# Performance work log

Measured on AMD Instinct MI355X. Metric: run time of the kernel, lower is better.

Reference implementation:

```python
import jax, jax.numpy as jnp
import numpy as np

VOCAB, EMB, HID = 32000, 256, 512
B, S = 16, 256


def setup_inputs() -> dict:
    key = jax.random.key(0)
    ks = jax.random.split(key, 7)
    x = jax.random.randint(ks[0], (B, S), 0, VOCAB, dtype=jnp.int32)
    E = jax.random.normal(ks[1], (VOCAB, EMB), dtype=jnp.float32) * 0.02
    # GRUCell kernels, gate order [z, r, h], reset_after=True (keras default)
    W = jax.random.normal(ks[2], (EMB, 3 * HID), dtype=jnp.float32) * 0.02
    U = jax.random.normal(ks[3], (HID, 3 * HID), dtype=jnp.float32) * 0.02
    b = jnp.zeros((2, 3 * HID), dtype=jnp.float32)  # [input_bias, recurrent_bias]
    Wd = jax.random.normal(ks[4], (HID, VOCAB), dtype=jnp.float32) * 0.02
    bd = jnp.zeros((VOCAB,), dtype=jnp.float32)
    return {"x": x, "E": E, "W": W, "U": U, "b": b, "Wd": Wd, "bd": bd}


def _gru_sequence(emb, W, U, b):
    # emb: [B, S, EMB]. Precompute all input-side gate projections at once.
    xw = jnp.einsum('bse,eh->bsh', emb, W) + b[0]          # [B, S, 3H]
    xw_t = jnp.transpose(xw, (1, 0, 2))                     # [S, B, 3H]
    b_rec = b[1]
    H = U.shape[0]

    def step(h, xt):
        rec = h @ U + b_rec                                 # [B, 3H]
        xz, xr, xh = xt[:, :H], xt[:, H:2 * H], xt[:, 2 * H:]
        rz, rr, rh = rec[:, :H], rec[:, H:2 * H], rec[:, 2 * H:]
        z = jax.nn.sigmoid(xz + rz)
        r = jax.nn.sigmoid(xr + rr)
        hh = jnp.tanh(xh + r * rh)                          # reset_after=True form
        h_new = z * h + (1.0 - z) * hh
        return h_new, h_new

    h0 = jnp.zeros((emb.shape[0], H), dtype=emb.dtype)
    _, hs = jax.lax.scan(step, h0, xw_t)                    # hs: [S, B, H]
    return jnp.transpose(hs, (1, 0, 2))                     # [B, S, H]


def reference(x, E, W, U, b, Wd, bd):
    emb = E[x]                                              # [B, S, EMB]
    h = _gru_sequence(emb, W, U, b)                         # [B, S, H]
    logits = jnp.einsum('bsh,hv->bsv', h, Wd) + bd          # [B, S, VOCAB]
    return logits
```

## Files before the change

kernel.cpp:

```cpp
#include <hip/hip_runtime.h>
#include <hip/hip_bf16.h>
#include <stdint.h>
#include <stddef.h>

#define NB 16
#define NS 256
#define NH 512
#define NE 256
#define NV 32000
#define NM (NB*NS)
#define N3H 1536

typedef __attribute__((ext_vector_type(8))) short short8v;
typedef __attribute__((ext_vector_type(4))) float float4v;
typedef __attribute__((address_space(1))) const unsigned int gas_u32;
typedef __attribute__((address_space(3))) unsigned int las_u32;

static __device__ __forceinline__ unsigned short f2bf(float f) {
  __hip_bfloat16 h = __float2bfloat16(f);
  return *reinterpret_cast<unsigned short*>(&h);
}
static __device__ __forceinline__ float bf2f(unsigned short u) {
  union { unsigned int u; float f; } c;
  c.u = ((unsigned int)u) << 16;
  return c.f;
}
static __device__ __forceinline__ float fast_tanh(float x) {
  float t = __expf(2.f * x);
  return (t - 1.f) / (t + 1.f);
}

__global__ void gather_emb(const int* __restrict__ x, const float* __restrict__ E,
                           unsigned short* __restrict__ A) {
  int m = blockIdx.x * 4 + (threadIdx.x >> 6);
  int lane = threadIdx.x & 63;
  int t = x[m];
  float4 v = reinterpret_cast<const float4*>(E + (size_t)t * NE)[lane];
  ushort4 o = make_ushort4(f2bf(v.x), f2bf(v.y), f2bf(v.z), f2bf(v.w));
  reinterpret_cast<ushort4*>(A + (size_t)m * NE)[lane] = o;
}

template<typename T>
__global__ void transpose_conv(const float* __restrict__ in, T* __restrict__ out,
                               int R, int C) {
  __shared__ float tile[32][33];
  int c0 = blockIdx.x * 32, r0 = blockIdx.y * 32;
  int tx = threadIdx.x, ty = threadIdx.y;
  #pragma unroll
  for (int i = 0; i < 32; i += 8)
    tile[ty + i][tx] = in[(size_t)(r0 + ty + i) * C + (c0 + tx)];
  __syncthreads();
  #pragma unroll
  for (int i = 0; i < 32; i += 8) {
    float v = tile[tx][ty + i];
    if constexpr (sizeof(T) == 2)
      out[(size_t)(c0 + ty + i) * R + (r0 + tx)] = (T)f2bf(v);
    else
      out[(size_t)(c0 + ty + i) * R + (r0 + tx)] = (T)v;
  }
}

template<bool OUT_BF16>
__launch_bounds__(256)
__global__ void gemm_bt(const unsigned short* __restrict__ A,
                        const unsigned short* __restrict__ BT,
                        const float* __restrict__ bias,
                        void* __restrict__ out, int N, int K) {
  __shared__ unsigned short As[128 * 32];
  __shared__ unsigned short Bs[128 * 32];
  const int tid = threadIdx.x;
  const int lane = tid & 63, wave = tid >> 6;
  const int wr = wave >> 1, wc = wave & 1;
  int nwg = gridDim.x * gridDim.y;
  int bid0 = blockIdx.y * gridDim.x + blockIdx.x;
  int q = nwg >> 3, r8 = nwg & 7;
  int xcd = bid0 & 7, idx = bid0 >> 3;
  int bid = (xcd < r8 ? xcd * (q + 1) : r8 * (q + 1) + (xcd - r8) * q) + idx;
  const int m0 = (bid / gridDim.x) * 128, n0 = (bid % gridDim.x) * 128;
  const int lr = lane & 15, lg = lane >> 4;
  float4v acc[4][4] = {};

  for (int k0 = 0; k0 < K; k0 += 32) {
    const char* Ab = (const char*)A;
    const char* Bb = (const char*)BT;
    #pragma unroll
    for (int qq = 0; qq < 2; ++qq) {
      int byteoff = qq * 4096 + tid * 16;
      int rr = byteoff >> 6, cb = byteoff & 63;
      const char* ga = Ab + ((size_t)(m0 + rr) * K + k0) * 2 + cb;
      const char* gb = Bb + ((size_t)(n0 + rr) * K + k0) * 2 + cb;
      char* la = (char*)As + qq * 4096 + wave * 1024;
      char* lb = (char*)Bs + qq * 4096 + wave * 1024;
      __builtin_amdgcn_global_load_lds((gas_u32*)ga, (las_u32*)la, 16, 0, 0);
      __builtin_amdgcn_global_load_lds((gas_u32*)gb, (las_u32*)lb, 16, 0, 0);
    }
    __syncthreads();
    short8v a[4], b[4];
    #pragma unroll
    for (int i = 0; i < 4; ++i)
      a[i] = *(const short8v*)((const char*)As + (wr * 64 + i * 16 + lr) * 64 + lg * 16);
    #pragma unroll
    for (int j = 0; j < 4; ++j)
      b[j] = *(const short8v*)((const char*)Bs + (wc * 64 + j * 16 + lr) * 64 + lg * 16);
    #pragma unroll
    for (int i = 0; i < 4; ++i) {
      #pragma unroll
      for (int j = 0; j < 4; ++j)
        acc[i][j] = __builtin_amdgcn_mfma_f32_16x16x32_bf16(a[i], b[j], acc[i][j], 0, 0, 0);
    }
    __syncthreads();
  }
  #pragma unroll
  for (int i = 0; i < 4; ++i) {
    int row = m0 + wr * 64 + i * 16 + lg * 4;
    #pragma unroll
    for (int j = 0; j < 4; ++j) {
      int col = n0 + wc * 64 + j * 16 + lr;
      float bv = bias[col];
      #pragma unroll
      for (int rr = 0; rr < 4; ++rr) {
        float v = acc[i][j][rr] + bv;
        if constexpr (OUT_BF16)
          ((unsigned short*)out)[(size_t)(row + rr) * N + col] = f2bf(v);
        else
          ((float*)out)[(size_t)(row + rr) * N + col] = v;
      }
    }
  }
}

#define SENT 0xFFFFFFFFu
__launch_bounds__(384, 1)
__global__ void gru_kernel(const unsigned short* __restrict__ xw,
                           const float* __restrict__ UT,
                           const float* __restrict__ bvec,
                           unsigned short* __restrict__ Hall,
                           unsigned int* __restrict__ Hex) {
  const int w = blockIdx.x, tid = threadIdx.x;
  const int grp = w >> 4;
  const int wq = w & 15;
  const int lane = tid & 63, wave = tid >> 6;
  const int lr = lane & 15, lg = lane >> 4;
  __shared__ unsigned short h_lds[4 * 512];
  __shared__ float red[4][100];

  int c = wave * 16 + lr;
  int g = c >> 5, dloc = c & 31;
  const float* up = UT + (size_t)(g * 512 + 32 * wq + dloc) * 512 + lg * 8;
  short8v Bf[16];
  #pragma unroll
  for (int kk = 0; kk < 16; ++kk) {
    float4 v0 = *(const float4*)(up + kk * 32);
    float4 v1 = *(const float4*)(up + kk * 32 + 4);
    short8v t;
    t[0] = (short)f2bf(v0.x); t[1] = (short)f2bf(v0.y);
    t[2] = (short)f2bf(v0.z); t[3] = (short)f2bf(v0.w);
    t[4] = (short)f2bf(v1.x); t[5] = (short)f2bf(v1.y);
    t[6] = (short)f2bf(v1.z); t[7] = (short)f2bf(v1.w);
    Bf[kk] = t;
  }
  for (int idx = tid; idx < 256; idx += 384)
    reinterpret_cast<uint4*>(h_lds)[idx] = make_uint4(0, 0, 0, 0);

  float h0 = 0.f, h1 = 0.f;
  float bz0 = 0, bz1 = 0, br0 = 0, br1 = 0, bh0 = 0, bh1 = 0;
  const int b_loc = tid >> 4, dp = tid & 15;
  const unsigned int* xp = nullptr;
  if (tid < 64) {
    const float* brec = bvec + 1536;
    int d = 32 * wq + 2 * dp;
    int b = grp * 4 + b_loc;
    bz0 = brec[d];        bz1 = brec[d + 1];
    br0 = brec[512 + d];  br1 = brec[513 + d];
    bh0 = brec[1024 + d]; bh1 = brec[1025 + d];
    xp = (const unsigned int*)xw + ((size_t)(b * 256) * 1536 + d) / 2;
  }
  const int pb = tid >> 6;
  const bool own = ((tid >> 2) & 15) == wq;
  __syncthreads();

  for (int s = 0; s < 256; ++s) {
    unsigned int xzw = 0, xrw = 0, xhw = 0;
    if (tid < 64) { xzw = xp[0]; xrw = xp[256]; xhw = xp[512]; xp += 768; }

    if (s > 0 && tid < 256 && !own) {
      const unsigned int* src = Hex + ((size_t)s * 4 + grp) * 1024 + tid * 4;
      unsigned int vv[4];
      #pragma unroll
      for (int i = 0; i < 4; ++i)
        vv[i] = __hip_atomic_load(&src[i], __ATOMIC_RELAXED, __HIP_MEMORY_SCOPE_AGENT);
      unsigned int pend = 0xF;
      while (pend) {
        unsigned int np = 0;
        #pragma unroll
        for (int i = 0; i < 4; ++i) if (pend & (1u << i)) {
          if (vv[i] != SENT) {
            int dpp = (tid & 63) * 4 + i;
            *(unsigned int*)((char*)h_lds + ((pb * 1024 + dpp * 4) ^ (pb << 4))) = vv[i];
          } else np |= 1u << i;
        }
        pend = np;
        if (pend) {
          __builtin_amdgcn_s_sleep(1);
          #pragma unroll
          for (int i = 0; i < 4; ++i) if (pend & (1u << i))
            vv[i] = __hip_atomic_load(&src[i], __ATOMIC_RELAXED, __HIP_MEMORY_SCOPE_AGENT);
        }
      }
    }
    __syncthreads();

    {
      float4v acc0 = {}, acc1 = {};
      #pragma unroll
      for (int kk = 0; kk < 16; ++kk) {
        int byteoff = ((lr & 3) * 1024 + kk * 64 + lg * 16) ^ ((lr & 3) << 4);
        short8v a = *(const short8v*)((const char*)h_lds + byteoff);
        if (kk & 1) acc1 = __builtin_amdgcn_mfma_f32_16x16x32_bf16(a, Bf[kk], acc1, 0, 0, 0);
        else        acc0 = __builtin_amdgcn_mfma_f32_16x16x32_bf16(a, Bf[kk], acc0, 0, 0, 0);
      }
      if (lg == 0) {
        #pragma unroll
        for (int rr = 0; rr < 4; ++rr)
          red[rr][c] = acc0[rr] + acc1[rr];
      }
    }
    __syncthreads();

    if (tid < 64) {
      float rz0 = red[b_loc][2 * dp],      rz1 = red[b_loc][2 * dp + 1];
      float rr0 = red[b_loc][32 + 2 * dp], rr1 = red[b_loc][33 + 2 * dp];
      float rh0 = red[b_loc][64 + 2 * dp], rh1 = red[b_loc][65 + 2 * dp];
      float xz0 = bf2f((unsigned short)(xzw & 0xffff)), xz1 = bf2f((unsigned short)(xzw >> 16));
      float xr0 = bf2f((unsigned short)(xrw & 0xffff)), xr1 = bf2f((unsigned short)(xrw >> 16));
      float xh0 = bf2f((unsigned short)(xhw & 0xffff)), xh1 = bf2f((unsigned short)(xhw >> 16));
      float z0 = 1.f / (1.f + __expf(-(xz0 + rz0 + bz0)));
      float z1 = 1.f / (1.f + __expf(-(xz1 + rz1 + bz1)));
      float r0 = 1.f / (1.f + __expf(-(xr0 + rr0 + br0)));
      float r1 = 1.f / (1.f + __expf(-(xr1 + rr1 + br1)));
      float hh0 = fast_tanh(xh0 + r0 * (rh0 + bh0));
      float hh1 = fast_tanh(xh1 + r1 * (rh1 + bh1));
      h0 = z0 * h0 + (1.f - z0) * hh0;
      h1 = z1 * h1 + (1.f - z1) * hh1;
      unsigned int pack = (unsigned int)f2bf(h0) | ((unsigned int)f2bf(h1) << 16);
      int dpp = wq * 16 + dp;
      __hip_atomic_store(&Hex[((size_t)(s + 1) * 4 + grp) * 1024 + b_loc * 256 + dpp], pack,
                         __ATOMIC_RELAXED, __HIP_MEMORY_SCOPE_AGENT);
      *(unsigned int*)((char*)h_lds + ((b_loc * 1024 + dpp * 4) ^ (b_loc << 4))) = pack;
      ((unsigned int*)Hall)[(size_t)((grp * 4 + b_loc) * 256 + s) * 256 + dpp] = pack;
    }
  }
}

extern "C" void kernel_launch(void* const* d_in, const int* in_sizes, int n_in,
                              void* d_out, int out_size, void* d_ws, size_t ws_size,
                              hipStream_t stream) {
  const int*   x  = (const int*)d_in[0];
  const float* E  = (const float*)d_in[1];
  const float* W  = (const float*)d_in[2];
  const float* U  = (const float*)d_in[3];
  const float* bv = (const float*)d_in[4];
  const float* Wd = (const float*)d_in[5];
  const float* bd = (const float*)d_in[6];
  float* out = (float*)d_out;

  char* ws = (char*)d_ws;
  size_t off = 0;
  auto alloc = [&](size_t bytes) -> void* {
    void* p = ws + off;
    off = (off + bytes + 255) & ~(size_t)255;
    return p;
  };
  unsigned short* Aemb = (unsigned short*)alloc((size_t)NM * NE * 2);
  unsigned short* WT   = (unsigned short*)alloc((size_t)N3H * NE * 2);
  float*          UT   = (float*)alloc((size_t)N3H * NH * 4);
  unsigned short* xwb  = (unsigned short*)alloc((size_t)NM * N3H * 2);
  unsigned short* WdT  = (unsigned short*)alloc((size_t)NV * NH * 2);
  unsigned short* Hall = (unsigned short*)alloc((size_t)NM * NH * 2);
  unsigned int*   Hex  = (unsigned int*)alloc((size_t)257 * 4096 * 4);

  hipMemsetAsync(Hex, 0xFF, (size_t)257 * 4096 * 4, stream);

  gather_emb<<<NM / 4, 256, 0, stream>>>(x, E, Aemb);
  transpose_conv<unsigned short><<<dim3(N3H / 32, NE / 32), dim3(32, 8), 0, stream>>>(W,  WT,  NE, N3H);
  transpose_conv<unsigned short><<<dim3(NV / 32,  NH / 32), dim3(32, 8), 0, stream>>>(Wd, WdT, NH, NV);
  transpose_conv<float>         <<<dim3(N3H / 32, NH / 32), dim3(32, 8), 0, stream>>>(U,  UT,  NH, N3H);

  gemm_bt<true><<<dim3(N3H / 128, NM / 128), 256, 0, stream>>>(Aemb, WT, bv, xwb, N3H, NE);

  gru_kernel<<<64, 384, 0, stream>>>(xwb, UT, bv, Hall, Hex);

  gemm_bt<false><<<dim3(NV / 128, NM / 128), 256, 0, stream>>>(Hall, WdT, bd, out, NV, NH);
}
```

Before: 812.9 us.

## Fuse GRU recurrence and vocab projection into one persistent producer-consumer kernel

Merges the sequential GRU kernel and the output-projection GEMM into a single launch. 64 workgroups run the recurrence and publish per-step progress counters, while 192 decoder workgroups wait on those counters and compute logits for 64-timestep chunks as soon as they are ready. The aim is to overlap the large vocab GEMM with the latency-bound recurrence. In exchange, the decoder uses smaller 64x128 tiles with no double buffering, which may run less efficiently than the standalone GEMM. It also relies on all 256 workgroups being co-resident to avoid deadlock, and the decoders' memory traffic may slow the recurrence.

```diff
diff --git a/kernel.cpp b/kernel.cpp
--- a/kernel.cpp
+++ b/kernel.cpp
@@ -10,6 +10,9 @@
 #define NV 32000
 #define NM (NB*NS)
 #define N3H 1536
+#define GRU_WGS 64
+#define DEC_WGS 192
+#define NCT 250
 
 typedef __attribute__((ext_vector_type(8))) short short8v;
 typedef __attribute__((ext_vector_type(4))) float float4v;
@@ -81,14 +84,12 @@
   float4v acc[4][4] = {};
 
   for (int k0 = 0; k0 < K; k0 += 32) {
-    const char* Ab = (const char*)A;
-    const char* Bb = (const char*)BT;
     #pragma unroll
     for (int qq = 0; qq < 2; ++qq) {
       int byteoff = qq * 4096 + tid * 16;
       int rr = byteoff >> 6, cb = byteoff & 63;
-      const char* ga = Ab + ((size_t)(m0 + rr) * K + k0) * 2 + cb;
-      const char* gb = Bb + ((size_t)(n0 + rr) * K + k0) * 2 + cb;
+      const char* ga = (const char*)A + ((size_t)(m0 + rr) * K + k0) * 2 + cb;
+      const char* gb = (const char*)BT + ((size_t)(n0 + rr) * K + k0) * 2 + cb;
       char* la = (char*)As + qq * 4096 + wave * 1024;
       char* lb = (char*)Bs + qq * 4096 + wave * 1024;
       __builtin_amdgcn_global_load_lds((gas_u32*)ga, (las_u32*)la, 16, 0, 0);
@@ -130,124 +131,214 @@
 }
 
 #define SENT 0xFFFFFFFFu
-__launch_bounds__(384, 1)
-__global__ void gru_kernel(const unsigned short* __restrict__ xw,
-                           const float* __restrict__ UT,
-                           const float* __restrict__ bvec,
-                           unsigned short* __restrict__ Hall,
-                           unsigned int* __restrict__ Hex) {
-  const int w = blockIdx.x, tid = threadIdx.x;
-  const int grp = w >> 4;
-  const int wq = w & 15;
+__launch_bounds__(512, 1)
+__global__ void fused_kernel(const unsigned short* __restrict__ xw,
+                             const float* __restrict__ UT,
+                             const float* __restrict__ bvec,
+                             const unsigned short* __restrict__ WdT,
+                             const float* __restrict__ bd,
+                             unsigned int* Hall,
+                             unsigned int* Hex,
+                             unsigned int* prog,
+                             float* out) {
+  const int tid = threadIdx.x;
   const int lane = tid & 63, wave = tid >> 6;
   const int lr = lane & 15, lg = lane >> 4;
-  __shared__ unsigned short h_lds[4 * 512];
-  __shared__ float red[4][100];
-
-  int c = wave * 16 + lr;
-  int g = c >> 5, dloc = c & 31;
-  const float* up = UT + (size_t)(g * 512 + 32 * wq + dloc) * 512 + lg * 8;
-  short8v Bf[16];
-  #pragma unroll
-  for (int kk = 0; kk < 16; ++kk) {
-    float4 v0 = *(const float4*)(up + kk * 32);
-    float4 v1 = *(const float4*)(up + kk * 32 + 4);
-    short8v t;
-    t[0] = (short)f2bf(v0.x); t[1] = (short)f2bf(v0.y);
-    t[2] = (short)f2bf(v0.z); t[3] = (short)f2bf(v0.w);
-    t[4] = (short)f2bf(v1.x); t[5] = (short)f2bf(v1.y);
-    t[6] = (short)f2bf(v1.z); t[7] = (short)f2bf(v1.w);
-    Bf[kk] = t;
-  }
-  for (int idx = tid; idx < 256; idx += 384)
-    reinterpret_cast<uint4*>(h_lds)[idx] = make_uint4(0, 0, 0, 0);
-
-  float h0 = 0.f, h1 = 0.f;
-  float bz0 = 0, bz1 = 0, br0 = 0, br1 = 0, bh0 = 0, bh1 = 0;
-  const int b_loc = tid >> 4, dp = tid & 15;
-  const unsigned int* xp = nullptr;
-  if (tid < 64) {
-    const float* brec = bvec + 1536;
-    int d = 32 * wq + 2 * dp;
-    int b = grp * 4 + b_loc;
-    bz0 = brec[d];        bz1 = brec[d + 1];
-    br0 = brec[512 + d];  br1 = brec[513 + d];
-    bh0 = brec[1024 + d]; bh1 = brec[1025 + d];
-    xp = (const unsigned int*)xw + ((size_t)(b * 256) * 1536 + d) / 2;
-  }
-  const int pb = tid >> 6;
-  const bool own = ((tid >> 2) & 15) == wq;
-  __syncthreads();
-
-  for (int s = 0; s < 256; ++s) {
-    unsigned int xzw = 0, xrw = 0, xhw = 0;
-    if (tid < 64) { xzw = xp[0]; xrw = xp[256]; xhw = xp[512]; xp += 768; }
-
-    if (s > 0 && tid < 256 && !own) {
-      const unsigned int* src = Hex + ((size_t)s * 4 + grp) * 1024 + tid * 4;
-      unsigned int vv[4];
-      #pragma unroll
-      for (int i = 0; i < 4; ++i)
-        vv[i] = __hip_atomic_load(&src[i], __ATOMIC_RELAXED, __HIP_MEMORY_SCOPE_AGENT);
-      unsigned int pend = 0xF;
-      while (pend) {
-        unsigned int np = 0;
-        #pragma unroll
-        for (int i = 0; i < 4; ++i) if (pend & (1u << i)) {
-          if (vv[i] != SENT) {
-            int dpp = (tid & 63) * 4 + i;
-            *(unsigned int*)((char*)h_lds + ((pb * 1024 + dpp * 4) ^ (pb << 4))) = vv[i];
-          } else np |= 1u << i;
-        }
-        pend = np;
-        if (pend) {
-          __builtin_amdgcn_s_sleep(1);
-          #pragma unroll
-          for (int i = 0; i < 4; ++i) if (pend & (1u << i))
-            vv[i] = __hip_atomic_load(&src[i], __ATOMIC_RELAXED, __HIP_MEMORY_SCOPE_AGENT);
-        }
-      }
-    }
-    __syncthreads();
-
-    {
-      float4v acc0 = {}, acc1 = {};
+  __shared__ __align__(16) char smem[12288];
+
+  if (blockIdx.x < GRU_WGS) {
+    __builtin_amdgcn_s_setprio(1);
+    unsigned short* h_lds = (unsigned short*)smem;
+    float (*red)[100] = (float(*)[100])(smem + 4096);
+    const int w = blockIdx.x;
+    const int grp = w >> 4;
+    const int wq = w & 15;
+
+    short8v Bf[16];
+    if (wave < 6) {
+      int c = wave * 16 + lr;
+      int g = c >> 5, dloc = c & 31;
+      const float* up = UT + (size_t)(g * 512 + 32 * wq + dloc) * 512 + lg * 8;
       #pragma unroll
       for (int kk = 0; kk < 16; ++kk) {
-        int byteoff = ((lr & 3) * 1024 + kk * 64 + lg * 16) ^ ((lr & 3) << 4);
-        short8v a = *(const short8v*)((const char*)h_lds + byteoff);
-        if (kk & 1) acc1 = __builtin_amdgcn_mfma_f32_16x16x32_bf16(a, Bf[kk], acc1, 0, 0, 0);
-        else        acc0 = __builtin_amdgcn_mfma_f32_16x16x32_bf16(a, Bf[kk], acc0, 0, 0, 0);
-      }
-      if (lg == 0) {
+        float4 v0 = *(const float4*)(up + kk * 32);
+        float4 v1 = *(const float4*)(up + kk * 32 + 4);
+        short8v t;
+        t[0] = (short)f2bf(v0.x); t[1] = (short)f2bf(v0.y);
+        t[2] = (short)f2bf(v0.z); t[3] = (short)f2bf(v0.w);
+        t[4] = (short)f2bf(v1.x); t[5] = (short)f2bf(v1.y);
+        t[6] = (short)f2bf(v1.z); t[7] = (short)f2bf(v1.w);
+        Bf[kk] = t;
+      }
+    }
+    for (int idx = tid; idx < 256; idx += 512)
+      reinterpret_cast<uint4*>(h_lds)[idx] = make_uint4(0, 0, 0, 0);
+
+    float h0 = 0.f, h1 = 0.f;
+    float bz0 = 0, bz1 = 0, br0 = 0, br1 = 0, bh0 = 0, bh1 = 0;
+    const int b_loc = tid >> 4, dp = tid & 15;
+    const unsigned int* xp = nullptr;
+    if (tid < 64) {
+      const float* brec = bvec + 1536;
+      int d = 32 * wq + 2 * dp;
+      int b = grp * 4 + b_loc;
+      bz0 = brec[d];        bz1 = brec[d + 1];
+      br0 = brec[512 + d];  br1 = brec[513 + d];
+      bh0 = brec[1024 + d]; bh1 = brec[1025 + d];
+      xp = (const unsigned int*)xw + ((size_t)(b * 256) * 1536 + d) / 2;
+    }
+    const int pb = tid >> 6;
+    const bool own = ((tid >> 2) & 15) == wq;
+    __syncthreads();
+
+    for (int s = 0; s < 256; ++s) {
+      unsigned int xzw = 0, xrw = 0, xhw = 0;
+      if (tid < 64) { xzw = xp[0]; xrw = xp[256]; xhw = xp[512]; xp += 768; }
+
+      if (s > 0 && tid < 256 && !own) {
+        const unsigned int* src = Hex + ((size_t)s * 4 + grp) * 1024 + tid * 4;
+        unsigned int vv[4];
         #pragma unroll
-        for (int rr = 0; rr < 4; ++rr)
-          red[rr][c] = acc0[rr] + acc1[rr];
-      }
-    }
-    __syncthreads();
-
-    if (tid < 64) {
-      float rz0 = red[b_loc][2 * dp],      rz1 = red[b_loc][2 * dp + 1];
-      float rr0 = red[b_loc][32 + 2 * dp], rr1 = red[b_loc][33 + 2 * dp];
-      float rh0 = red[b_loc][64 + 2 * dp], rh1 = red[b_loc][65 + 2 * dp];
-      float xz0 = bf2f((unsigned short)(xzw & 0xffff)), xz1 = bf2f((unsigned short)(xzw >> 16));
-      float xr0 = bf2f((unsigned short)(xrw & 0xffff)), xr1 = bf2f((unsigned short)(xrw >> 16));
-      float xh0 = bf2f((unsigned short)(xhw & 0xffff)), xh1 = bf2f((unsigned short)(xhw >> 16));
-      float z0 = 1.f / (1.f + __expf(-(xz0 + rz0 + bz0)));
-      float z1 = 1.f / (1.f + __expf(-(xz1 + rz1 + bz1)));
-      float r0 = 1.f / (1.f + __expf(-(xr0 + rr0 + br0)));
-      float r1 = 1.f / (1.f + __expf(-(xr1 + rr1 + br1)));
-      float hh0 = fast_tanh(xh0 + r0 * (rh0 + bh0));
-      float hh1 = fast_tanh(xh1 + r1 * (rh1 + bh1));
-      h0 = z0 * h0 + (1.f - z0) * hh0;
-      h1 = z1 * h1 + (1.f - z1) * hh1;
-      unsigned int pack = (unsigned int)f2bf(h0) | ((unsigned int)f2bf(h1) << 16);
-      int dpp = wq * 16 + dp;
-      __hip_atomic_store(&Hex[((size_t)(s + 1) * 4 + grp) * 1024 + b_loc * 256 + dpp], pack,
-                         __ATOMIC_RELAXED, __HIP_MEMORY_SCOPE_AGENT);
-      *(unsigned int*)((char*)h_lds + ((b_loc * 1024 + dpp * 4) ^ (b_loc << 4))) = pack;
-      ((unsigned int*)Hall)[(size_t)((grp * 4 + b_loc) * 256 + s) * 256 + dpp] = pack;
+        for (int i = 0; i < 4; ++i)
+          vv[i] = __hip_atomic_load(&src[i], __ATOMIC_RELAXED, __HIP_MEMORY_SCOPE_AGENT);
+        unsigned int pend = 0xF;
+        while (pend) {
+          unsigned int np = 0;
+          #pragma unroll
+          for (int i = 0; i < 4; ++i) if (pend & (1u << i)) {
+            if (vv[i] != SENT) {
+              int dpp = (tid & 63) * 4 + i;
+              *(unsigned int*)((char*)h_lds + ((pb * 1024 + dpp * 4) ^ (pb << 4))) = vv[i];
+            } else np |= 1u << i;
+          }
+          pend = np;
+          if (pend) {
+            __builtin_amdgcn_s_sleep(1);
+            #pragma unroll
+            for (int i = 0; i < 4; ++i) if (pend & (1u << i))
+              vv[i] = __hip_atomic_load(&src[i], __ATOMIC_RELAXED, __HIP_MEMORY_SCOPE_AGENT);
+          }
+        }
+      }
+      __syncthreads();
+
+      if (wave < 6) {
+        float4v acc0 = {}, acc1 = {};
+        #pragma unroll
+        for (int kk = 0; kk < 16; ++kk) {
+          int byteoff = ((lr & 3) * 1024 + kk * 64 + lg * 16) ^ ((lr & 3) << 4);
+          short8v a = *(const short8v*)((const char*)h_lds + byteoff);
+          if (kk & 1) acc1 = __builtin_amdgcn_mfma_f32_16x16x32_bf16(a, Bf[kk], acc1, 0, 0, 0);
+          else        acc0 = __builtin_amdgcn_mfma_f32_16x16x32_bf16(a, Bf[kk], acc0, 0, 0, 0);
+        }
+        if (lg == 0) {
+          int c = wave * 16 + lr;
+          #pragma unroll
+          for (int rr = 0; rr < 4; ++rr)
+            red[rr][c] = acc0[rr] + acc1[rr];
+        }
+      }
+      __syncthreads();
+
+      if (tid < 64) {
+        float rz0 = red[b_loc][2 * dp],      rz1 = red[b_loc][2 * dp + 1];
+        float rr0 = red[b_loc][32 + 2 * dp], rr1 = red[b_loc][33 + 2 * dp];
+        float rh0 = red[b_loc][64 + 2 * dp], rh1 = red[b_loc][65 + 2 * dp];
+        float xz0 = bf2f((unsigned short)(xzw & 0xffff)), xz1 = bf2f((unsigned short)(xzw >> 16));
+        float xr0 = bf2f((unsigned short)(xrw & 0xffff)), xr1 = bf2f((unsigned short)(xrw >> 16));
+        float xh0 = bf2f((unsigned short)(xhw & 0xffff)), xh1 = bf2f((unsigned short)(xhw >> 16));
+        float z0 = 1.f / (1.f + __expf(-(xz0 + rz0 + bz0)));
+        float z1 = 1.f / (1.f + __expf(-(xz1 + rz1 + bz1)));
+        float r0 = 1.f / (1.f + __expf(-(xr0 + rr0 + br0)));
+        float r1 = 1.f / (1.f + __expf(-(xr1 + rr1 + br1)));
+        float hh0 = fast_tanh(xh0 + r0 * (rh0 + bh0));
+        float hh1 = fast_tanh(xh1 + r1 * (rh1 + bh1));
+        h0 = z0 * h0 + (1.f - z0) * hh0;
+        h1 = z1 * h1 + (1.f - z1) * hh1;
+        unsigned int pack = (unsigned int)f2bf(h0) | ((unsigned int)f2bf(h1) << 16);
+        int dpp = wq * 16 + dp;
+        __hip_atomic_store(&Hex[((size_t)(s + 1) * 4 + grp) * 1024 + b_loc * 256 + dpp], pack,
+                           __ATOMIC_RELAXED, __HIP_MEMORY_SCOPE_AGENT);
+        *(unsigned int*)((char*)h_lds + ((b_loc * 1024 + dpp * 4) ^ (b_loc << 4))) = pack;
+        __hip_atomic_store(&Hall[(size_t)((grp * 4 + b_loc) * 256 + s) * 256 + dpp], pack,
+                           __ATOMIC_RELAXED, __HIP_MEMORY_SCOPE_AGENT);
+        if (tid == 0)
+          __hip_atomic_fetch_add(&prog[grp * 256 + s], 1u,
+                                 __ATOMIC_RELEASE, __HIP_MEMORY_SCOPE_AGENT);
+      }
+    }
+  } else {
+    unsigned short* As = (unsigned short*)smem;
+    unsigned short* Bs = (unsigned short*)(smem + 4096);
+    const int d = blockIdx.x - GRU_WGS;
+    const int wr = wave >> 2, wc = wave & 3;
+
+    for (int sc = 0; sc < 4; ++sc) {
+      const int s_need = sc * 64 + 63;
+      unsigned ready = 0;
+      for (int ct = d; ct < NCT; ct += DEC_WGS) {
+        const int n0 = ct * 128;
+        for (int b = 0; b < NB; ++b) {
+          const int g = b >> 2;
+          if (!(ready & (1u << g))) {
+            if (tid == 0) {
+              const unsigned int* pp = &prog[g * 256 + s_need];
+              while (__hip_atomic_load(pp, __ATOMIC_RELAXED, __HIP_MEMORY_SCOPE_AGENT) < 16u)
+                __builtin_amdgcn_s_sleep(8);
+              (void)__hip_atomic_load(pp, __ATOMIC_ACQUIRE, __HIP_MEMORY_SCOPE_AGENT);
+            }
+            __syncthreads();
+            ready |= 1u << g;
+          }
+          const int m0 = b * 256 + sc * 64;
+          float4v acc[2][2] = {};
+          for (int k0 = 0; k0 < NH; k0 += 32) {
+            if (tid < 256) {
+              #pragma unroll
+              for (int qq = 0; qq < 2; ++qq) {
+                int off = qq * 4096 + tid * 16;
+                int row = off >> 6, cb = off & 63;
+                const char* gb = (const char*)WdT + (size_t)(n0 + row) * 1024 + k0 * 2 + cb;
+                char* lb = (char*)Bs + qq * 4096 + wave * 1024;
+                __builtin_amdgcn_global_load_lds((gas_u32*)gb, (las_u32*)lb, 16, 0, 0);
+              }
+            } else {
+              int off = (tid - 256) * 16;
+              int row = off >> 6, cb = off & 63;
+              const char* ga = (const char*)Hall + (size_t)(m0 + row) * 1024 + k0 * 2 + cb;
+              char* la = (char*)As + (wave - 4) * 1024;
+              __builtin_amdgcn_global_load_lds((gas_u32*)ga, (las_u32*)la, 16, 0, 0);
+            }
+            __syncthreads();
+            short8v a[2], bb[2];
+            #pragma unroll
+            for (int i = 0; i < 2; ++i)
+              a[i] = *(const short8v*)((const char*)As + (wr * 32 + i * 16 + lr) * 64 + lg * 16);
+            #pragma unroll
+            for (int j = 0; j < 2; ++j)
+              bb[j] = *(const short8v*)((const char*)Bs + (wc * 32 + j * 16 + lr) * 64 + lg * 16);
+            #pragma unroll
+            for (int i = 0; i < 2; ++i) {
+              #pragma unroll
+              for (int j = 0; j < 2; ++j)
+                acc[i][j] = __builtin_amdgcn_mfma_f32_16x16x32_bf16(a[i], bb[j], acc[i][j], 0, 0, 0);
+            }
+            __syncthreads();
+          }
+          #pragma unroll
+          for (int i = 0; i < 2; ++i) {
+            int row = m0 + wr * 32 + i * 16 + lg * 4;
+            #pragma unroll
+            for (int j = 0; j < 2; ++j) {
+              int col = n0 + wc * 32 + j * 16 + lr;
+              float bv = bd[col];
+              #pragma unroll
+              for (int rr = 0; rr < 4; ++rr)
+                out[(size_t)(row + rr) * NV + col] = acc[i][j][rr] + bv;
+            }
+          }
+        }
+      }
     }
   }
 }
@@ -276,10 +367,12 @@
   float*          UT   = (float*)alloc((size_t)N3H * NH * 4);
   unsigned short* xwb  = (unsigned short*)alloc((size_t)NM * N3H * 2);
   unsigned short* WdT  = (unsigned short*)alloc((size_t)NV * NH * 2);
-  unsigned short* Hall = (unsigned short*)alloc((size_t)NM * NH * 2);
+  unsigned int*   Hall = (unsigned int*)alloc((size_t)NM * NH * 2);
   unsigned int*   Hex  = (unsigned int*)alloc((size_t)257 * 4096 * 4);
+  unsigned int*   prog = (unsigned int*)alloc((size_t)4 * 256 * 4);
 
   hipMemsetAsync(Hex, 0xFF, (size_t)257 * 4096 * 4, stream);
+  hipMemsetAsync(prog, 0, (size_t)4 * 256 * 4, stream);
 
   gather_emb<<<NM / 4, 256, 0, stream>>>(x, E, Aemb);
   transpose_conv<unsigned short><<<dim3(N3H / 32, NE / 32), dim3(32, 8), 0, stream>>>(W,  WT,  NE, N3H);
@@ -288,7 +381,6 @@
 
   gemm_bt<true><<<dim3(N3H / 128, NM / 128), 256, 0, stream>>>(Aemb, WT, bv, xwb, N3H, NE);
 
-  gru_kernel<<<64, 384, 0, stream>>>(xwb, UT, bv, Hall, Hex);
-
-  gemm_bt<false><<<dim3(NV / 128, NM / 128), 256, 0, stream>>>(Hall, WdT, bd, out, NV, NH);
-}
+  fused_kernel<<<GRU_WGS + DEC_WGS, 512, 0, stream>>>(xwb, UT, bv, WdT, bd,
+                                                      Hall, Hex, prog, out);
+}
```

Result: slower. 1.541 ms (+89.5%).

## Restructure GRU step to 4 waves with double-buffered h and decode straight from Hex

Applied to the files above, without the earlier changes.

The recurrent kernel moves from 6 waves to 4. Each wave holds two B-fragment sets covering its 8 output columns across all three gates, and the per-wave gate math uses a scratch buffer plus a lane shuffle, which removes one block-wide barrier per step. The hidden-state LDS buffer is double-buffered and the exchange polling now uses 64-bit loads. The separate Hall store is dropped, and a dedicated decoder GEMM reads the hidden states directly from the Hex exchange buffer with non-temporal output stores. This trades more registers and more MFMA work per wave for fewer barriers on the serial critical path and less global write traffic.

```diff
diff --git a/kernel.cpp b/kernel.cpp
--- a/kernel.cpp
+++ b/kernel.cpp
@@ -81,14 +81,12 @@
   float4v acc[4][4] = {};
 
   for (int k0 = 0; k0 < K; k0 += 32) {
-    const char* Ab = (const char*)A;
-    const char* Bb = (const char*)BT;
     #pragma unroll
     for (int qq = 0; qq < 2; ++qq) {
       int byteoff = qq * 4096 + tid * 16;
       int rr = byteoff >> 6, cb = byteoff & 63;
-      const char* ga = Ab + ((size_t)(m0 + rr) * K + k0) * 2 + cb;
-      const char* gb = Bb + ((size_t)(n0 + rr) * K + k0) * 2 + cb;
+      const char* ga = (const char*)A + ((size_t)(m0 + rr) * K + k0) * 2 + cb;
+      const char* gb = (const char*)BT + ((size_t)(n0 + rr) * K + k0) * 2 + cb;
       char* la = (char*)As + qq * 4096 + wave * 1024;
       char* lb = (char*)Bs + qq * 4096 + wave * 1024;
       __builtin_amdgcn_global_load_lds((gas_u32*)ga, (las_u32*)la, 16, 0, 0);
@@ -130,124 +128,195 @@
 }
 
 #define SENT 0xFFFFFFFFu
-__launch_bounds__(384, 1)
+__launch_bounds__(256, 1)
 __global__ void gru_kernel(const unsigned short* __restrict__ xw,
                            const float* __restrict__ UT,
                            const float* __restrict__ bvec,
-                           unsigned short* __restrict__ Hall,
                            unsigned int* __restrict__ Hex) {
-  const int w = blockIdx.x, tid = threadIdx.x;
-  const int grp = w >> 4;
-  const int wq = w & 15;
-  const int lane = tid & 63, wave = tid >> 6;
+  const int blk = blockIdx.x, tid = threadIdx.x;
+  const int grp = blk >> 4, wq = blk & 15;
+  const int lane = tid & 63, w = tid >> 6;
   const int lr = lane & 15, lg = lane >> 4;
-  __shared__ unsigned short h_lds[4 * 512];
-  __shared__ float red[4][100];
-
-  int c = wave * 16 + lr;
-  int g = c >> 5, dloc = c & 31;
-  const float* up = UT + (size_t)(g * 512 + 32 * wq + dloc) * 512 + lg * 8;
-  short8v Bf[16];
-  #pragma unroll
-  for (int kk = 0; kk < 16; ++kk) {
-    float4 v0 = *(const float4*)(up + kk * 32);
-    float4 v1 = *(const float4*)(up + kk * 32 + 4);
-    short8v t;
-    t[0] = (short)f2bf(v0.x); t[1] = (short)f2bf(v0.y);
-    t[2] = (short)f2bf(v0.z); t[3] = (short)f2bf(v0.w);
-    t[4] = (short)f2bf(v1.x); t[5] = (short)f2bf(v1.y);
-    t[6] = (short)f2bf(v1.z); t[7] = (short)f2bf(v1.w);
-    Bf[kk] = t;
-  }
-  for (int idx = tid; idx < 256; idx += 384)
-    reinterpret_cast<uint4*>(h_lds)[idx] = make_uint4(0, 0, 0, 0);
-
-  float h0 = 0.f, h1 = 0.f;
-  float bz0 = 0, bz1 = 0, br0 = 0, br1 = 0, bh0 = 0, bh1 = 0;
-  const int b_loc = tid >> 4, dp = tid & 15;
+  __shared__ __align__(16) unsigned short h_lds[2][4 * 512];
+  __shared__ __align__(16) float scratch[4][96];
+
+  const int D0 = 32 * wq;
+  short8v Bf0[16], Bf1[16];
+  {
+    int dloc = D0 + 8 * w + (lr & 7);
+    int colg0 = (lr < 8) ? dloc : (512 + dloc);
+    const float* u0 = UT + (size_t)colg0 * 512 + lg * 8;
+    const float* u1 = UT + (size_t)(1024 + dloc) * 512 + lg * 8;
+    #pragma unroll
+    for (int kk = 0; kk < 16; ++kk) {
+      float4 a0 = *(const float4*)(u0 + kk * 32);
+      float4 a1 = *(const float4*)(u0 + kk * 32 + 4);
+      float4 c0 = *(const float4*)(u1 + kk * 32);
+      float4 c1 = *(const float4*)(u1 + kk * 32 + 4);
+      short8v t0, t1;
+      t0[0] = (short)f2bf(a0.x); t0[1] = (short)f2bf(a0.y);
+      t0[2] = (short)f2bf(a0.z); t0[3] = (short)f2bf(a0.w);
+      t0[4] = (short)f2bf(a1.x); t0[5] = (short)f2bf(a1.y);
+      t0[6] = (short)f2bf(a1.z); t0[7] = (short)f2bf(a1.w);
+      t1[0] = (short)f2bf(c0.x); t1[1] = (short)f2bf(c0.y);
+      t1[2] = (short)f2bf(c0.z); t1[3] = (short)f2bf(c0.w);
+      t1[4] = (short)f2bf(c1.x); t1[5] = (short)f2bf(c1.y);
+      t1[6] = (short)f2bf(c1.z); t1[7] = (short)f2bf(c1.w);
+      Bf0[kk] = t0; Bf1[kk] = t1;
+    }
+  }
+  for (int i = tid; i < 512; i += 256)
+    reinterpret_cast<uint4*>(h_lds)[i] = make_uint4(0, 0, 0, 0);
+
+  const int b = lane & 3, di = lane >> 2;
+  const int d = D0 + 8 * w + di;
+  const int hi = di & 1;
+  float h_old = 0.f, bz = 0.f, br = 0.f, bh = 0.f;
   const unsigned int* xp = nullptr;
-  if (tid < 64) {
+  if (lane < 32) {
     const float* brec = bvec + 1536;
-    int d = 32 * wq + 2 * dp;
-    int b = grp * 4 + b_loc;
-    bz0 = brec[d];        bz1 = brec[d + 1];
-    br0 = brec[512 + d];  br1 = brec[513 + d];
-    bh0 = brec[1024 + d]; bh1 = brec[1025 + d];
-    xp = (const unsigned int*)xw + ((size_t)(b * 256) * 1536 + d) / 2;
-  }
-  const int pb = tid >> 6;
+    bz = brec[d]; br = brec[512 + d]; bh = brec[1024 + d];
+    xp = (const unsigned int*)xw + (size_t)(grp * 4 + b) * 256 * 768 + ((d & ~1) >> 1);
+  }
   const bool own = ((tid >> 2) & 15) == wq;
+  const int pbb = tid >> 6;
   __syncthreads();
 
+  int p = 0;
   for (int s = 0; s < 256; ++s) {
     unsigned int xzw = 0, xrw = 0, xhw = 0;
-    if (tid < 64) { xzw = xp[0]; xrw = xp[256]; xhw = xp[512]; xp += 768; }
-
-    if (s > 0 && tid < 256 && !own) {
-      const unsigned int* src = Hex + ((size_t)s * 4 + grp) * 1024 + tid * 4;
-      unsigned int vv[4];
-      #pragma unroll
-      for (int i = 0; i < 4; ++i)
-        vv[i] = __hip_atomic_load(&src[i], __ATOMIC_RELAXED, __HIP_MEMORY_SCOPE_AGENT);
-      unsigned int pend = 0xF;
+    if (lane < 32) { xzw = xp[0]; xrw = xp[256]; xhw = xp[512]; xp += 768; }
+
+    if (s > 0 && !own) {
+      const unsigned long long* src =
+          (const unsigned long long*)(Hex + ((size_t)s * 4 + grp) * 1024 + tid * 4);
+      unsigned long long v0 = __hip_atomic_load(&src[0], __ATOMIC_RELAXED, __HIP_MEMORY_SCOPE_AGENT);
+      unsigned long long v1 = __hip_atomic_load(&src[1], __ATOMIC_RELAXED, __HIP_MEMORY_SCOPE_AGENT);
+      unsigned int pend = 3;
+      char* dst = (char*)h_lds[p];
+      int dpp = (tid & 63) * 4;
       while (pend) {
         unsigned int np = 0;
-        #pragma unroll
-        for (int i = 0; i < 4; ++i) if (pend & (1u << i)) {
-          if (vv[i] != SENT) {
-            int dpp = (tid & 63) * 4 + i;
-            *(unsigned int*)((char*)h_lds + ((pb * 1024 + dpp * 4) ^ (pb << 4))) = vv[i];
-          } else np |= 1u << i;
+        if (pend & 1) {
+          if ((unsigned int)v0 != SENT && (unsigned int)(v0 >> 32) != SENT)
+            *(unsigned long long*)(dst + ((pbb * 1024 + dpp * 4) ^ (pbb << 4))) = v0;
+          else np |= 1;
+        }
+        if (pend & 2) {
+          if ((unsigned int)v1 != SENT && (unsigned int)(v1 >> 32) != SENT)
+            *(unsigned long long*)(dst + ((pbb * 1024 + (dpp + 2) * 4) ^ (pbb << 4))) = v1;
+          else np |= 2;
         }
         pend = np;
         if (pend) {
           __builtin_amdgcn_s_sleep(1);
-          #pragma unroll
-          for (int i = 0; i < 4; ++i) if (pend & (1u << i))
-            vv[i] = __hip_atomic_load(&src[i], __ATOMIC_RELAXED, __HIP_MEMORY_SCOPE_AGENT);
+          if (pend & 1) v0 = __hip_atomic_load(&src[0], __ATOMIC_RELAXED, __HIP_MEMORY_SCOPE_AGENT);
+          if (pend & 2) v1 = __hip_atomic_load(&src[1], __ATOMIC_RELAXED, __HIP_MEMORY_SCOPE_AGENT);
         }
       }
     }
     __syncthreads();
 
-    {
-      float4v acc0 = {}, acc1 = {};
+    float4v acc0 = {}, acc1 = {};
+    const char* hb = (const char*)h_lds[p];
+    #pragma unroll
+    for (int kk = 0; kk < 16; ++kk) {
+      int off = ((lane & 3) * 1024 + kk * 64 + lg * 16) ^ ((lane & 3) << 4);
+      short8v a = *(const short8v*)(hb + off);
+      acc0 = __builtin_amdgcn_mfma_f32_16x16x32_bf16(a, Bf0[kk], acc0, 0, 0, 0);
+      acc1 = __builtin_amdgcn_mfma_f32_16x16x32_bf16(a, Bf1[kk], acc1, 0, 0, 0);
+    }
+    if (lg == 0) {
+      *(float4*)&scratch[w][lr * 4] = *(float4*)&acc0;
+      if (lr < 8)
+        *(float4*)&scratch[w][64 + lr * 4] = *(float4*)&acc1;
+    }
+    if (lane < 32) {
+      float rz = scratch[w][lane];
+      float rr = scratch[w][32 + lane];
+      float rh = scratch[w][64 + lane];
+      float xz = bf2f((unsigned short)(hi ? (xzw >> 16) : (xzw & 0xffff)));
+      float xr = bf2f((unsigned short)(hi ? (xrw >> 16) : (xrw & 0xffff)));
+      float xh = bf2f((unsigned short)(hi ? (xhw >> 16) : (xhw & 0xffff)));
+      float z = 1.f / (1.f + __expf(-(xz + rz + bz)));
+      float r = 1.f / (1.f + __expf(-(xr + rr + br)));
+      float hh = fast_tanh(xh + r * (rh + bh));
+      h_old = z * h_old + (1.f - z) * hh;
+      unsigned int mine = f2bf(h_old);
+      unsigned int part = (unsigned int)__shfl_xor((int)mine, 4);
+      if ((lane & 4) == 0) {
+        unsigned int pack = mine | (part << 16);
+        int wordi = b * 256 + wq * 16 + w * 4 + (di >> 1);
+        __hip_atomic_store(&Hex[(size_t)(s + 1) * 4096 + grp * 1024 + wordi], pack,
+                           __ATOMIC_RELAXED, __HIP_MEMORY_SCOPE_AGENT);
+        *(unsigned int*)((char*)h_lds[p ^ 1] +
+                         ((b * 1024 + (wordi & 255) * 4) ^ (b << 4))) = pack;
+      }
+    }
+    p ^= 1;
+  }
+}
+
+__launch_bounds__(256)
+__global__ void dec_gemm(const char* __restrict__ HexB,
+                         const unsigned short* __restrict__ WdT,
+                         const float* __restrict__ bd,
+                         float* __restrict__ out) {
+  __shared__ unsigned short As[128 * 32];
+  __shared__ unsigned short Bs[128 * 32];
+  const int tid = threadIdx.x;
+  const int lane = tid & 63, wave = tid >> 6;
+  const int wr = wave >> 1, wc = wave & 1;
+  const int lr = lane & 15, lg = lane >> 4;
+  int bid0 = blockIdx.x;
+  int bid = (bid0 & 7) * 1000 + (bid0 >> 3);
+  const int mt = bid & 31, nt = bid >> 5;
+  const int b = mt >> 1, s0 = (mt & 1) * 128;
+  const int n0 = nt * 128;
+  float4v acc[4][4] = {};
+
+  for (int k0 = 0; k0 < NH; k0 += 32) {
+    #pragma unroll
+    for (int qq = 0; qq < 2; ++qq) {
+      int off = qq * 4096 + tid * 16;
+      int rloc = off >> 6, cb = off & 63;
+      int s = s0 + rloc;
+      const char* ga = HexB + ((size_t)(s + 1) * 4 + (b >> 2)) * 4096 +
+                       (size_t)(b & 3) * 1024 + k0 * 2 + cb;
+      const char* gb = (const char*)WdT + ((size_t)(n0 + rloc) * 512 + k0) * 2 + cb;
+      __builtin_amdgcn_global_load_lds((gas_u32*)ga,
+          (las_u32*)((char*)As + qq * 4096 + wave * 1024), 16, 0, 0);
+      __builtin_amdgcn_global_load_lds((gas_u32*)gb,
+          (las_u32*)((char*)Bs + qq * 4096 + wave * 1024), 16, 0, 0);
+    }
+    __syncthreads();
+    short8v a[4], bb[4];
+    #pragma unroll
+    for (int i = 0; i < 4; ++i)
+      a[i] = *(const short8v*)((const char*)As + (wr * 64 + i * 16 + lr) * 64 + lg * 16);
+    #pragma unroll
+    for (int j = 0; j < 4; ++j)
+      bb[j] = *(const short8v*)((const char*)Bs + (wc * 64 + j * 16 + lr) * 64 + lg * 16);
+    #pragma unroll
+    for (int i = 0; i < 4; ++i) {
       #pragma unroll
-      for (int kk = 0; kk < 16; ++kk) {
-        int byteoff = ((lr & 3) * 1024 + kk * 64 + lg * 16) ^ ((lr & 3) << 4);
-        short8v a = *(const short8v*)((const char*)h_lds + byteoff);
-        if (kk & 1) acc1 = __builtin_amdgcn_mfma_f32_16x16x32_bf16(a, Bf[kk], acc1, 0, 0, 0);
-        else        acc0 = __builtin_amdgcn_mfma_f32_16x16x32_bf16(a, Bf[kk], acc0, 0, 0, 0);
+      for (int j = 0; j < 4; ++j)
+        acc[i][j] = __builtin_amdgcn_mfma_f32_16x16x32_bf16(a[i], bb[j], acc[i][j], 0, 0, 0);
+    }
+    __syncthreads();
+  }
+  #pragma unroll
+  for (int i = 0; i < 4; ++i) {
+    int l = wr * 64 + i * 16 + lg * 4;
+    #pragma unroll
+    for (int j = 0; j < 4; ++j) {
+      int col = n0 + wc * 64 + j * 16 + lr;
+      float bv = bd[col];
+      #pragma unroll
+      for (int rr = 0; rr < 4; ++rr) {
+        size_t m = (size_t)(b * 256 + s0 + l + rr);
+        __builtin_nontemporal_store(acc[i][j][rr] + bv, &out[m * NV + col]);
       }
-      if (lg == 0) {
-        #pragma unroll
-        for (int rr = 0; rr < 4; ++rr)
-          red[rr][c] = acc0[rr] + acc1[rr];
-      }
-    }
-    __syncthreads();
-
-    if (tid < 64) {
-      float rz0 = red[b_loc][2 * dp],      rz1 = red[b_loc][2 * dp + 1];
-      float rr0 = red[b_loc][32 + 2 * dp], rr1 = red[b_loc][33 + 2 * dp];
-      float rh0 = red[b_loc][64 + 2 * dp], rh1 = red[b_loc][65 + 2 * dp];
-      float xz0 = bf2f((unsigned short)(xzw & 0xffff)), xz1 = bf2f((unsigned short)(xzw >> 16));
-      float xr0 = bf2f((unsigned short)(xrw & 0xffff)), xr1 = bf2f((unsigned short)(xrw >> 16));
-      float xh0 = bf2f((unsigned short)(xhw & 0xffff)), xh1 = bf2f((unsigned short)(xhw >> 16));
-      float z0 = 1.f / (1.f + __expf(-(xz0 + rz0 + bz0)));
-      float z1 = 1.f / (1.f + __expf(-(xz1 + rz1 + bz1)));
-      float r0 = 1.f / (1.f + __expf(-(xr0 + rr0 + br0)));
-      float r1 = 1.f / (1.f + __expf(-(xr1 + rr1 + br1)));
-      float hh0 = fast_tanh(xh0 + r0 * (rh0 + bh0));
-      float hh1 = fast_tanh(xh1 + r1 * (rh1 + bh1));
-      h0 = z0 * h0 + (1.f - z0) * hh0;
-      h1 = z1 * h1 + (1.f - z1) * hh1;
-      unsigned int pack = (unsigned int)f2bf(h0) | ((unsigned int)f2bf(h1) << 16);
-      int dpp = wq * 16 + dp;
-      __hip_atomic_store(&Hex[((size_t)(s + 1) * 4 + grp) * 1024 + b_loc * 256 + dpp], pack,
-                         __ATOMIC_RELAXED, __HIP_MEMORY_SCOPE_AGENT);
-      *(unsigned int*)((char*)h_lds + ((b_loc * 1024 + dpp * 4) ^ (b_loc << 4))) = pack;
-      ((unsigned int*)Hall)[(size_t)((grp * 4 + b_loc) * 256 + s) * 256 + dpp] = pack;
     }
   }
 }
@@ -276,19 +345,18 @@
   float*          UT   = (float*)alloc((size_t)N3H * NH * 4);
   unsigned short* xwb  = (unsigned short*)alloc((size_t)NM * N3H * 2);
   unsigned short* WdT  = (unsigned short*)alloc((size_t)NV * NH * 2);
-  unsigned short* Hall = (unsigned short*)alloc((size_t)NM * NH * 2);
   unsigned int*   Hex  = (unsigned int*)alloc((size_t)257 * 4096 * 4);
 
   hipMemsetAsync(Hex, 0xFF, (size_t)257 * 4096 * 4, stream);
 
   gather_emb<<<NM / 4, 256, 0, stream>>>(x, E, Aemb);
   transpose_conv<unsigned short><<<dim3(N3H / 32, NE / 32), dim3(32, 8), 0, stream>>>(W,  WT,  NE, N3H);
+  transpose_conv<float>         <<<dim3(N3H / 32, NH / 32), dim3(32, 8), 0, stream>>>(U,  UT,  NH, N3H);
   transpose_conv<unsigned short><<<dim3(NV / 32,  NH / 32), dim3(32, 8), 0, stream>>>(Wd, WdT, NH, NV);
-  transpose_conv<float>         <<<dim3(N3H / 32, NH / 32), dim3(32, 8), 0, stream>>>(U,  UT,  NH, N3H);
 
   gemm_bt<true><<<dim3(N3H / 128, NM / 128), 256, 0, stream>>>(Aemb, WT, bv, xwb, N3H, NE);
 
-  gru_kernel<<<64, 384, 0, stream>>>(xwb, UT, bv, Hall, Hex);
-
-  gemm_bt<false><<<dim3(NV / 128, NM / 128), 256, 0, stream>>>(Hall, WdT, bd, out, NV, NH);
-}
+  gru_kernel<<<64, 256, 0, stream>>>(xwb, UT, bv, Hex);
+
+  dec_gemm<<<8000, 256, 0, stream>>>((const char*)Hex, WdT, bd, out);
+}
```

Result: faster. 688.1 us (-15.4%).
